# Kernel optimization log

Measured on AMD Instinct MI355X. Metric: run time of the kernel, lower is better.

The kernel has to match this reference:

```python
import jax, jax.numpy as jnp
import numpy as np


def setup_inputs() -> dict:
    key = jax.random.key(0)
    kq, kk, kv = jax.random.split(key, 3)
    B, H, N, D = 4, 16, 2048, 64
    q = jax.random.normal(kq, (B, H, N, D), dtype=jnp.float32)
    k = jax.random.normal(kk, (B, N, D), dtype=jnp.float32)
    v = jax.random.normal(kv, (B, N, D), dtype=jnp.float32)
    return {"q": q, "k": k, "v": v}


def reference(q, k, v):
    # q: [B,H,N,D], k/v: [B,N,D] (KV shared across heads)
    scale = q.shape[-1] ** -0.5
    sim = jnp.einsum('bhid,bjd->bhij', q, k) * scale  # [B,H,N,N]
    attn = jax.nn.softmax(sim, axis=-1)
    return jnp.einsum('bhij,bjd->bhid', attn, v)  # [B,H,N,D]
```

## Files before the change

kernel.cpp:

```cpp
#include <hip/hip_runtime.h>
#include <hip/hip_bf16.h>

#define B_ 4
#define H_ 16
#define N_ 2048
#define D_ 64
#define BM 128
#define BN 64

typedef __bf16 bf16;
typedef bf16 bf16x4 __attribute__((ext_vector_type(4)));
typedef bf16 bf16x8 __attribute__((ext_vector_type(8)));
typedef float f32x2 __attribute__((ext_vector_type(2)));
typedef float f32x16 __attribute__((ext_vector_type(16)));
typedef unsigned u32x2 __attribute__((ext_vector_type(2)));
typedef unsigned u32x4 __attribute__((ext_vector_type(4)));

#define SCALE_LOG2E 0.18033688011112042f

#define GBL(p) ((const __attribute__((address_space(1))) void*)(p))
#define LDS(p) ((__attribute__((address_space(3))) void*)(p))

__global__ __launch_bounds__(512) void convert_kv(const float* __restrict__ k,
                                                  const float* __restrict__ v,
                                                  bf16* __restrict__ img) {
    __shared__ bf16 VT[64][66];
    const int tile = blockIdx.x;
    const int b = tile >> 5, T = tile & 31;
    const int t = threadIdx.x;
    bf16* timg = img + (size_t)tile * 8192;

    const int mtks = t >> 6;
    const int ln   = t & 63;
    const int mt = mtks >> 2, ks = mtks & 3;

    {
        const int kvr = T * 64 + mt * 32 + (ln & 31);
        const int d0  = ks * 16 + (ln >> 5) * 8;
        const float* src = k + ((size_t)b * N_ + kvr) * D_ + d0;
        float4 a = *(const float4*)src;
        float4 c = *(const float4*)(src + 4);
        bf16x8 o;
        o[0] = (bf16)a.x; o[1] = (bf16)a.y; o[2] = (bf16)a.z; o[3] = (bf16)a.w;
        o[4] = (bf16)c.x; o[5] = (bf16)c.y; o[6] = (bf16)c.z; o[7] = (bf16)c.w;
        *(bf16x8*)(timg + t * 8) = o;
    }

    {
        const int kv = t >> 3;
        const int c8 = (t & 7) * 8;
        const float* src = v + ((size_t)b * N_ + T * 64 + kv) * D_ + c8;
        float4 a = *(const float4*)src;
        float4 c = *(const float4*)(src + 4);
        VT[kv][c8 + 0] = (bf16)a.x; VT[kv][c8 + 1] = (bf16)a.y;
        VT[kv][c8 + 2] = (bf16)a.z; VT[kv][c8 + 3] = (bf16)a.w;
        VT[kv][c8 + 4] = (bf16)c.x; VT[kv][c8 + 5] = (bf16)c.y;
        VT[kv][c8 + 6] = (bf16)c.z; VT[kv][c8 + 7] = (bf16)c.w;
    }
    __syncthreads();
    {
        const int d   = mt * 32 + (ln & 31);
        const int kv0 = ks * 16 + (ln >> 5) * 8;
        bf16x8 o;
        #pragma unroll
        for (int j = 0; j < 8; ++j) o[j] = VT[kv0 + j][d];
        *(bf16x8*)(timg + 4096 + t * 8) = o;
    }
}

static __device__ inline bf16x4 pack4(float a, float b, float c, float d) {
    bf16x4 r; r[0] = (bf16)a; r[1] = (bf16)b; r[2] = (bf16)c; r[3] = (bf16)d; return r;
}

static __device__ inline bf16x8 cswap(bf16x4 lo, bf16x4 hi) {
    u32x2 l = __builtin_bit_cast(u32x2, lo);
    u32x2 h = __builtin_bit_cast(u32x2, hi);
    u32x2 r0 = __builtin_amdgcn_permlane32_swap(l[0], h[0], false, false);
    u32x2 r1 = __builtin_amdgcn_permlane32_swap(l[1], h[1], false, false);
    u32x4 o; o[0] = r0[0]; o[1] = r1[0]; o[2] = r0[1]; o[3] = r1[1];
    return __builtin_bit_cast(bf16x8, o);
}

__global__ __launch_bounds__(512, 4) void attn_fwd(const float* __restrict__ q,
                                                   const bf16* __restrict__ img,
                                                   float* __restrict__ out) {
    __shared__ __align__(16) bf16 KV[2][2][8192];
    __shared__ float EXL[4][64];

    const int tid  = threadIdx.x;
    const int lane = tid & 63;
    const int wv   = tid >> 6;
    const int grp  = wv >> 2;
    const int wp   = wv & 3;
    const int half = lane >> 5;
    const int l31  = lane & 31;

    const int bh = blockIdx.y;
    const int b  = bh >> 4;
    const int q0 = blockIdx.x * BM + wp * 32;

    const bf16* tiles = img + (size_t)b * 32 * 8192;

    bf16x8 qf[4];
    #pragma unroll
    for (int ks = 0; ks < 4; ++ks) {
        const float* src = q + ((size_t)bh * N_ + q0 + l31) * D_ + ks * 16 + half * 8;
        float4 a = *(const float4*)src;
        float4 c = *(const float4*)(src + 4);
        bf16x8 pk;
        pk[0] = (bf16)(a.x * SCALE_LOG2E); pk[1] = (bf16)(a.y * SCALE_LOG2E);
        pk[2] = (bf16)(a.z * SCALE_LOG2E); pk[3] = (bf16)(a.w * SCALE_LOG2E);
        pk[4] = (bf16)(c.x * SCALE_LOG2E); pk[5] = (bf16)(c.y * SCALE_LOG2E);
        pk[6] = (bf16)(c.z * SCALE_LOG2E); pk[7] = (bf16)(c.w * SCALE_LOG2E);
        qf[ks] = pk;
    }

    f32x16 acc[2] = {{}, {}};
    float lacc = 0.f;

    auto issue_dma = [&](int t, int p) {
        const bf16* g = tiles + (size_t)t * 8192;
        #pragma unroll
        for (int j = 0; j < 4; ++j) {
            const int c = wp * 4 + j;
            __builtin_amdgcn_global_load_lds(GBL(g + c * 512 + lane * 8),
                                             LDS(&KV[grp][p][c * 512]), 16, 0, 0);
        }
    };

    const int t0 = grp * 16;
    issue_dma(t0, 0);

    for (int it = 0; it < 16; ++it) {
        const int p = it & 1;
        __syncthreads();
        if (it + 1 < 16) issue_dma(t0 + it + 1, p ^ 1);

        f32x16 s[2] = {{}, {}};
        __builtin_amdgcn_s_setprio(1);
        #pragma unroll
        for (int ks = 0; ks < 4; ++ks) {
            bf16x8 k0 = *(const bf16x8*)&KV[grp][p][((0 * 4 + ks) * 64 + lane) * 8];
            bf16x8 k1 = *(const bf16x8*)&KV[grp][p][((1 * 4 + ks) * 64 + lane) * 8];
            s[0] = __builtin_amdgcn_mfma_f32_32x32x16_bf16(k0, qf[ks], s[0], 0, 0, 0);
            s[1] = __builtin_amdgcn_mfma_f32_32x32x16_bf16(k1, qf[ks], s[1], 0, 0, 0);
        }
        __builtin_amdgcn_s_setprio(0);
        #pragma unroll
        for (int mt = 0; mt < 2; ++mt) {
            float pv[16];
            #pragma unroll
            for (int r = 0; r < 16; ++r) pv[r] = __builtin_amdgcn_exp2f(s[mt][r]);
            float t0s = 0.f, t1s = 0.f;
            #pragma unroll
            for (int r = 0; r < 8; ++r) { t0s += pv[r]; t1s += pv[8 + r]; }
            lacc += t0s + t1s;
            #pragma unroll
            for (int sp = 0; sp < 2; ++sp) {
                bf16x4 lo = pack4(pv[8 * sp + 0], pv[8 * sp + 1], pv[8 * sp + 2], pv[8 * sp + 3]);
                bf16x4 hi = pack4(pv[8 * sp + 4], pv[8 * sp + 5], pv[8 * sp + 6], pv[8 * sp + 7]);
                bf16x8 bfrag = cswap(lo, hi);
                const int g = mt * 2 + sp;
                bf16x8 v0 = *(const bf16x8*)&KV[grp][p][4096 + ((0 * 4 + g) * 64 + lane) * 8];
                bf16x8 v1 = *(const bf16x8*)&KV[grp][p][4096 + ((1 * 4 + g) * 64 + lane) * 8];
                __builtin_amdgcn_s_setprio(1);
                acc[0] = __builtin_amdgcn_mfma_f32_32x32x16_bf16(v0, bfrag, acc[0], 0, 0, 0);
                acc[1] = __builtin_amdgcn_mfma_f32_32x32x16_bf16(v1, bfrag, acc[1], 0, 0, 0);
                __builtin_amdgcn_s_setprio(0);
            }
        }
    }

    __syncthreads();
    float* ex = (float*)&KV[0][0][0] + wp * 2048;

    if (grp == 1) {
        #pragma unroll
        for (int mt = 0; mt < 2; ++mt)
            #pragma unroll
            for (int rq = 0; rq < 4; ++rq) {
                const int c = mt * 4 + rq;
                float4 v4;
                v4.x = acc[mt][4 * rq + 0];
                v4.y = acc[mt][4 * rq + 1];
                v4.z = acc[mt][4 * rq + 2];
                v4.w = acc[mt][4 * rq + 3];
                *(float4*)&ex[(c * 64 + lane) * 4] = v4;
            }
        EXL[wp][lane] = lacc;
    }
    __syncthreads();
    if (grp == 0) {
        lacc += EXL[wp][lane];
        #pragma unroll
        for (int mt = 0; mt < 2; ++mt)
            #pragma unroll
            for (int rq = 0; rq < 4; ++rq) {
                const int c = mt * 4 + rq;
                float4 v4 = *(const float4*)&ex[(c * 64 + lane) * 4];
                acc[mt][4 * rq + 0] += v4.x;
                acc[mt][4 * rq + 1] += v4.y;
                acc[mt][4 * rq + 2] += v4.z;
                acc[mt][4 * rq + 3] += v4.w;
            }

        float l = lacc + __shfl_xor(lacc, 32);
        float inv = 1.0f / l;
        const int qrow = q0 + l31;
        float* dst = out + ((size_t)bh * N_ + qrow) * D_ + 4 * half;
        #pragma unroll
        for (int mt = 0; mt < 2; ++mt)
            #pragma unroll
            for (int rq = 0; rq < 4; ++rq) {
                float4 o;
                o.x = acc[mt][4 * rq + 0] * inv;
                o.y = acc[mt][4 * rq + 1] * inv;
                o.z = acc[mt][4 * rq + 2] * inv;
                o.w = acc[mt][4 * rq + 3] * inv;
                *(float4*)(dst + mt * 32 + 8 * rq) = o;
            }
    }
}

extern "C" void kernel_launch(void* const* d_in, const int* in_sizes, int n_in,
                              void* d_out, int out_size, void* d_ws, size_t ws_size,
                              hipStream_t stream) {
    const float* q = (const float*)d_in[0];
    const float* k = (const float*)d_in[1];
    const float* v = (const float*)d_in[2];
    float* out = (float*)d_out;

    bf16* img = (bf16*)d_ws;

    convert_kv<<<B_ * 32, 512, 0, stream>>>(k, v, img);
    dim3 grid(N_ / BM, B_ * H_);
    attn_fwd<<<grid, 512, 0, stream>>>(q, img, out);
}
```

Measured before the change: 158.4 us.

## Load K/V fragments directly from global memory into registers, drop LDS staging

Removes the LDS double-buffered DMA staging and the two-group KV split with its cross-group reduction. Each of four waves now walks all 32 KV tiles, loading K and V MFMA fragments straight from global memory into registers. This removes block-wide barriers, LDS traffic and the final reduction, at the cost of more global/L2 reads per wave, no load-compute overlap beyond what the compiler schedules, and half the waves per block.

```diff
diff --git a/kernel.cpp b/kernel.cpp
--- a/kernel.cpp
+++ b/kernel.cpp
@@ -6,20 +6,15 @@
 #define N_ 2048
 #define D_ 64
 #define BM 128
-#define BN 64
 
 typedef __bf16 bf16;
 typedef bf16 bf16x4 __attribute__((ext_vector_type(4)));
 typedef bf16 bf16x8 __attribute__((ext_vector_type(8)));
-typedef float f32x2 __attribute__((ext_vector_type(2)));
 typedef float f32x16 __attribute__((ext_vector_type(16)));
 typedef unsigned u32x2 __attribute__((ext_vector_type(2)));
 typedef unsigned u32x4 __attribute__((ext_vector_type(4)));
 
 #define SCALE_LOG2E 0.18033688011112042f
-
-#define GBL(p) ((const __attribute__((address_space(1))) void*)(p))
-#define LDS(p) ((__attribute__((address_space(3))) void*)(p))
 
 __global__ __launch_bounds__(512) void convert_kv(const float* __restrict__ k,
                                                   const float* __restrict__ v,
@@ -81,23 +76,18 @@
     return __builtin_bit_cast(bf16x8, o);
 }
 
-__global__ __launch_bounds__(512, 4) void attn_fwd(const float* __restrict__ q,
+__global__ __launch_bounds__(256, 4) void attn_fwd(const float* __restrict__ q,
                                                    const bf16* __restrict__ img,
                                                    float* __restrict__ out) {
-    __shared__ __align__(16) bf16 KV[2][2][8192];
-    __shared__ float EXL[4][64];
-
     const int tid  = threadIdx.x;
     const int lane = tid & 63;
     const int wv   = tid >> 6;
-    const int grp  = wv >> 2;
-    const int wp   = wv & 3;
     const int half = lane >> 5;
     const int l31  = lane & 31;
 
     const int bh = blockIdx.y;
     const int b  = bh >> 4;
-    const int q0 = blockIdx.x * BM + wp * 32;
+    const int q0 = blockIdx.x * BM + wv * 32;
 
     const bf16* tiles = img + (size_t)b * 32 * 8192;
 
@@ -118,34 +108,26 @@
     f32x16 acc[2] = {{}, {}};
     float lacc = 0.f;
 
-    auto issue_dma = [&](int t, int p) {
-        const bf16* g = tiles + (size_t)t * 8192;
+    for (int it = 0; it < 32; ++it) {
+        const bf16* tp = tiles + (size_t)it * 8192;
+
+        bf16x8 kf[8];
         #pragma unroll
-        for (int j = 0; j < 4; ++j) {
-            const int c = wp * 4 + j;
-            __builtin_amdgcn_global_load_lds(GBL(g + c * 512 + lane * 8),
-                                             LDS(&KV[grp][p][c * 512]), 16, 0, 0);
-        }
-    };
-
-    const int t0 = grp * 16;
-    issue_dma(t0, 0);
-
-    for (int it = 0; it < 16; ++it) {
-        const int p = it & 1;
-        __syncthreads();
-        if (it + 1 < 16) issue_dma(t0 + it + 1, p ^ 1);
+        for (int u = 0; u < 8; ++u)
+            kf[u] = *(const bf16x8*)(tp + ((size_t)(u * 64 + lane)) * 8);
 
         f32x16 s[2] = {{}, {}};
-        __builtin_amdgcn_s_setprio(1);
         #pragma unroll
         for (int ks = 0; ks < 4; ++ks) {
-            bf16x8 k0 = *(const bf16x8*)&KV[grp][p][((0 * 4 + ks) * 64 + lane) * 8];
-            bf16x8 k1 = *(const bf16x8*)&KV[grp][p][((1 * 4 + ks) * 64 + lane) * 8];
-            s[0] = __builtin_amdgcn_mfma_f32_32x32x16_bf16(k0, qf[ks], s[0], 0, 0, 0);
-            s[1] = __builtin_amdgcn_mfma_f32_32x32x16_bf16(k1, qf[ks], s[1], 0, 0, 0);
+            s[0] = __builtin_amdgcn_mfma_f32_32x32x16_bf16(kf[0 * 4 + ks], qf[ks], s[0], 0, 0, 0);
+            s[1] = __builtin_amdgcn_mfma_f32_32x32x16_bf16(kf[1 * 4 + ks], qf[ks], s[1], 0, 0, 0);
         }
-        __builtin_amdgcn_s_setprio(0);
+
+        bf16x8 vf[8];
+        #pragma unroll
+        for (int u = 0; u < 8; ++u)
+            vf[u] = *(const bf16x8*)(tp + 4096 + ((size_t)(u * 64 + lane)) * 8);
+
         #pragma unroll
         for (int mt = 0; mt < 2; ++mt) {
             float pv[16];
@@ -161,65 +143,27 @@
                 bf16x4 hi = pack4(pv[8 * sp + 4], pv[8 * sp + 5], pv[8 * sp + 6], pv[8 * sp + 7]);
                 bf16x8 bfrag = cswap(lo, hi);
                 const int g = mt * 2 + sp;
-                bf16x8 v0 = *(const bf16x8*)&KV[grp][p][4096 + ((0 * 4 + g) * 64 + lane) * 8];
-                bf16x8 v1 = *(const bf16x8*)&KV[grp][p][4096 + ((1 * 4 + g) * 64 + lane) * 8];
-                __builtin_amdgcn_s_setprio(1);
-                acc[0] = __builtin_amdgcn_mfma_f32_32x32x16_bf16(v0, bfrag, acc[0], 0, 0, 0);
-                acc[1] = __builtin_amdgcn_mfma_f32_32x32x16_bf16(v1, bfrag, acc[1], 0, 0, 0);
-                __builtin_amdgcn_s_setprio(0);
+                acc[0] = __builtin_amdgcn_mfma_f32_32x32x16_bf16(vf[0 * 4 + g], bfrag, acc[0], 0, 0, 0);
+                acc[1] = __builtin_amdgcn_mfma_f32_32x32x16_bf16(vf[1 * 4 + g], bfrag, acc[1], 0, 0, 0);
             }
         }
     }
 
-    __syncthreads();
-    float* ex = (float*)&KV[0][0][0] + wp * 2048;
-
-    if (grp == 1) {
+    float l = lacc + __shfl_xor(lacc, 32);
+    float inv = 1.0f / l;
+    const int qrow = q0 + l31;
+    float* dst = out + ((size_t)bh * N_ + qrow) * D_ + 4 * half;
+    #pragma unroll
+    for (int mt = 0; mt < 2; ++mt)
         #pragma unroll
-        for (int mt = 0; mt < 2; ++mt)
-            #pragma unroll
-            for (int rq = 0; rq < 4; ++rq) {
-                const int c = mt * 4 + rq;
-                float4 v4;
-                v4.x = acc[mt][4 * rq + 0];
-                v4.y = acc[mt][4 * rq + 1];
-                v4.z = acc[mt][4 * rq + 2];
-                v4.w = acc[mt][4 * rq + 3];
-                *(float4*)&ex[(c * 64 + lane) * 4] = v4;
-            }
-        EXL[wp][lane] = lacc;
-    }
-    __syncthreads();
-    if (grp == 0) {
-        lacc += EXL[wp][lane];
-        #pragma unroll
-        for (int mt = 0; mt < 2; ++mt)
-            #pragma unroll
-            for (int rq = 0; rq < 4; ++rq) {
-                const int c = mt * 4 + rq;
-                float4 v4 = *(const float4*)&ex[(c * 64 + lane) * 4];
-                acc[mt][4 * rq + 0] += v4.x;
-                acc[mt][4 * rq + 1] += v4.y;
-                acc[mt][4 * rq + 2] += v4.z;
-                acc[mt][4 * rq + 3] += v4.w;
-            }
-
-        float l = lacc + __shfl_xor(lacc, 32);
-        float inv = 1.0f / l;
-        const int qrow = q0 + l31;
-        float* dst = out + ((size_t)bh * N_ + qrow) * D_ + 4 * half;
-        #pragma unroll
-        for (int mt = 0; mt < 2; ++mt)
-            #pragma unroll
-            for (int rq = 0; rq < 4; ++rq) {
-                float4 o;
-                o.x = acc[mt][4 * rq + 0] * inv;
-                o.y = acc[mt][4 * rq + 1] * inv;
-                o.z = acc[mt][4 * rq + 2] * inv;
-                o.w = acc[mt][4 * rq + 3] * inv;
-                *(float4*)(dst + mt * 32 + 8 * rq) = o;
-            }
-    }
+        for (int rq = 0; rq < 4; ++rq) {
+            float4 o;
+            o.x = acc[mt][4 * rq + 0] * inv;
+            o.y = acc[mt][4 * rq + 1] * inv;
+            o.z = acc[mt][4 * rq + 2] * inv;
+            o.w = acc[mt][4 * rq + 3] * inv;
+            *(float4*)(dst + mt * 32 + 8 * rq) = o;
+        }
 }
 
 extern "C" void kernel_launch(void* const* d_in, const int* in_sizes, int n_in,
@@ -234,5 +178,5 @@
 
     convert_kv<<<B_ * 32, 512, 0, stream>>>(k, v, img);
     dim3 grid(N_ / BM, B_ * H_);
-    attn_fwd<<<grid, 512, 0, stream>>>(q, img, out);
+    attn_fwd<<<grid, 256, 0, stream>>>(q, img, out);
 }
```

Measured after the change: 164.0 us. +3.5%, slower.
